# Optimization experiments

Measured on AMD Instinct MI355X. Metric: run time of the kernel, lower is better.

## Reference

```python
import jax, jax.numpy as jnp
import numpy as np

N_NODES = 5200    # max node index bounded by EW_weight length (5200)
N_INCID = 5200    # hyperedge_index.size(1), bounded by EW_weight length
N_HEDGES = 1000   # bounded by hyperedge_weight parameter length
N_DIM = 4096
NEG_SLOPE = 0.01  # torch.nn.LeakyReLU() default


def setup_inputs() -> dict:
    key = jax.random.key(0)
    k1, k2, k3, k4, k5, k6 = jax.random.split(key, 6)
    node_idx = jax.random.randint(k1, (N_INCID,), 0, N_NODES, dtype=jnp.int32)
    edge_idx = jax.random.randint(k2, (N_INCID,), 0, N_HEDGES, dtype=jnp.int32)
    edge_idx = edge_idx.at[-1].set(N_HEDGES - 1)  # ensure num_edges = max+1 = N_HEDGES (static)
    hyperedge_index = jnp.stack([node_idx, edge_idx], axis=0)
    features = jax.random.normal(k3, (N_NODES, N_DIM), dtype=jnp.float32)
    hyperedge_type = jnp.round(jax.random.uniform(k4, (N_HEDGES, 1), dtype=jnp.float32))
    return {
        "features": features,
        "hyperedge_index": hyperedge_index,
        "hyperedge_type": hyperedge_type,
        "hyperedge_weight": jnp.ones((1000,), jnp.float32),
        "hyperedge_attr1": jax.random.uniform(k5, (N_DIM,), dtype=jnp.float32),
        "hyperedge_attr2": jax.random.uniform(k6, (N_DIM,), dtype=jnp.float32),
        "EW_weight": jnp.ones((5200,), jnp.float32),
        "bias": jnp.zeros((N_DIM,), jnp.float32),
    }


def reference(features, hyperedge_index, hyperedge_type, hyperedge_weight,
              hyperedge_attr1, hyperedge_attr2, EW_weight, bias):
    node_idx = hyperedge_index[0]  # [E] node index of each incidence
    edge_idx = hyperedge_index[1]  # [E] hyperedge index of each incidence
    E = node_idx.shape[0]

    hw = hyperedge_weight[:N_HEDGES]   # hgnn slices param to num_edges
    norm = EW_weight[:E]               # hgnn slices param to E, passed as EW_weight

    # hyperedge_attr is computed but unused (use_attention=False in source)
    _ = hyperedge_attr1 * hyperedge_type + hyperedge_attr2 * (1.0 - hyperedge_type)

    # D: node-degree normalization (sum of incident hyperedge weights per node)
    D = jax.ops.segment_sum(hw[edge_idx], node_idx, num_segments=N_NODES)
    Dinv = jnp.where(D == 0, 0.0, 1.0 / D)
    # B: hyperedge normalization (sum of EW weights of member nodes per edge)
    B = jax.ops.segment_sum(norm[node_idx], edge_idx, num_segments=N_HEDGES)
    Binv = jnp.where(B == 0, 0.0, 1.0 / B)

    # Stage 1: node -> hyperedge (flow source_to_target), message = B_e * x_v
    msg1 = Binv[edge_idx][:, None] * features[node_idx]           # [E, F]
    edge_out = jax.ops.segment_sum(msg1, edge_idx, num_segments=N_HEDGES)  # [num_edges, F]

    # Stage 2: hyperedge -> node (flow target_to_source), message = D_v * e_feat
    msg2 = Dinv[node_idx][:, None] * edge_out[edge_idx]           # [E, F]
    node_out = jax.ops.segment_sum(msg2, node_idx, num_segments=N_NODES)   # [N, F]

    node_out = node_out + bias
    return (jax.nn.leaky_relu(node_out, NEG_SLOPE),
            jax.nn.leaky_relu(edge_out, NEG_SLOPE))
```

## Files before the change

### kernel.cpp

```cpp
#include <hip/hip_runtime.h>

#define NN 5200
#define NI 5200
#define NH 1000
#define ND 4096
#define SLOPE 0.01f


__global__ void count_k(const int* __restrict__ hidx, int* __restrict__ ecnt,
                        int* __restrict__ ncnt) {
    int i = blockIdx.x * blockDim.x + threadIdx.x;
    if (i < NI) {
        atomicAdd(&ncnt[hidx[i]], 1);
        atomicAdd(&ecnt[hidx[NI + i]], 1);
    }
}

__device__ void scan_one(const int* __restrict__ cnt, int* __restrict__ off,
                         int* __restrict__ fill, int n, int* lds) {
    int t = threadIdx.x;
    int per = (n + 1023) >> 10;
    int base = t * per;
    int s = 0;
    for (int i = 0; i < per; ++i) {
        int id = base + i;
        if (id < n) s += cnt[id];
    }
    lds[t] = s;
    __syncthreads();
    for (int d = 1; d < 1024; d <<= 1) {
        int v = (t >= d) ? lds[t - d] : 0;
        __syncthreads();
        lds[t] += v;
        __syncthreads();
    }
    int total = lds[1023];
    int run = (t == 0) ? 0 : lds[t - 1];
    for (int i = 0; i < per; ++i) {
        int id = base + i;
        if (id < n) { off[id] = run; fill[id] = run; run += cnt[id]; }
    }
    if (t == 0) off[n] = total;
}

__global__ void __launch_bounds__(1024) scan_k(const int* ecnt, const int* ncnt,
                                               int* eoff, int* noff,
                                               int* efill, int* nfill) {
    __shared__ int lds[1024];
    scan_one(ecnt, eoff, efill, NH, lds);
    __syncthreads();
    scan_one(ncnt, noff, nfill, NN, lds);
}

__global__ void scatter_k(const int* __restrict__ hidx, int* __restrict__ efill,
                          int* __restrict__ nfill, int* __restrict__ elist,
                          int* __restrict__ nlist) {
    int i = blockIdx.x * blockDim.x + threadIdx.x;
    if (i < NI) {
        int p = atomicAdd(&nfill[hidx[i]], 1);
        nlist[p] = i;
        int q = atomicAdd(&efill[hidx[NI + i]], 1);
        elist[q] = i;
    }
}


__global__ void __launch_bounds__(256) edge_k(const float* __restrict__ feat,
        const int* __restrict__ hidx, const float* __restrict__ eww,
        const int* __restrict__ eoff, const int* __restrict__ elist,
        float* __restrict__ eraw) {
    int h = blockIdx.x, t = threadIdx.x;
    int s = eoff[h], e = eoff[h + 1];
    __shared__ float sBinv;
    if (t == 0) {
        float B = 0.f;
        for (int i = s; i < e; ++i) B += eww[hidx[elist[i]]];
        sBinv = (B == 0.f) ? 0.f : 1.f / B;
    }
    __syncthreads();
    float binv = sBinv;
    float4 a0 = make_float4(0, 0, 0, 0), a1 = a0, a2 = a0, a3 = a0;
    for (int i = s; i < e; ++i) {
        const float4* row = (const float4*)(feat + (size_t)hidx[elist[i]] * ND);
        float4 v0 = row[t], v1 = row[t + 256], v2 = row[t + 512], v3 = row[t + 768];
        a0.x += v0.x; a0.y += v0.y; a0.z += v0.z; a0.w += v0.w;
        a1.x += v1.x; a1.y += v1.y; a1.z += v1.z; a1.w += v1.w;
        a2.x += v2.x; a2.y += v2.y; a2.z += v2.z; a2.w += v2.w;
        a3.x += v3.x; a3.y += v3.y; a3.z += v3.z; a3.w += v3.w;
    }
    a0.x *= binv; a0.y *= binv; a0.z *= binv; a0.w *= binv;
    a1.x *= binv; a1.y *= binv; a1.z *= binv; a1.w *= binv;
    a2.x *= binv; a2.y *= binv; a2.z *= binv; a2.w *= binv;
    a3.x *= binv; a3.y *= binv; a3.z *= binv; a3.w *= binv;
    float4* out = (float4*)(eraw + (size_t)h * ND);
    out[t] = a0; out[t + 256] = a1; out[t + 512] = a2; out[t + 768] = a3;
}

__global__ void __launch_bounds__(256) node_k(const float* __restrict__ eraw,
        const int* __restrict__ hidx, const float* __restrict__ hw,
        const float* __restrict__ bias, const int* __restrict__ noff,
        const int* __restrict__ nlist, float* __restrict__ nout) {
    int n = blockIdx.x, t = threadIdx.x;
    int s = noff[n], e = noff[n + 1];
    __shared__ float sDinv;
    if (t == 0) {
        float D = 0.f;
        for (int i = s; i < e; ++i) D += hw[hidx[NI + nlist[i]]];
        sDinv = (D == 0.f) ? 0.f : 1.f / D;
    }
    __syncthreads();
    float dinv = sDinv;
    float4 a0 = make_float4(0, 0, 0, 0), a1 = a0, a2 = a0, a3 = a0;
    for (int i = s; i < e; ++i) {
        const float4* row = (const float4*)(eraw + (size_t)hidx[NI + nlist[i]] * ND);
        float4 v0 = row[t], v1 = row[t + 256], v2 = row[t + 512], v3 = row[t + 768];
        a0.x += v0.x; a0.y += v0.y; a0.z += v0.z; a0.w += v0.w;
        a1.x += v1.x; a1.y += v1.y; a1.z += v1.z; a1.w += v1.w;
        a2.x += v2.x; a2.y += v2.y; a2.z += v2.z; a2.w += v2.w;
        a3.x += v3.x; a3.y += v3.y; a3.z += v3.z; a3.w += v3.w;
    }
    const float4* b4 = (const float4*)bias;
    float4* out = (float4*)(nout + (size_t)n * ND);
#define FIN(ak, idx)                                                     \
    {                                                                    \
        float4 b = b4[idx];                                              \
        float4 v;                                                        \
        v.x = dinv * ak.x + b.x; v.y = dinv * ak.y + b.y;                \
        v.z = dinv * ak.z + b.z; v.w = dinv * ak.w + b.w;                \
        v.x = v.x >= 0.f ? v.x : SLOPE * v.x;                            \
        v.y = v.y >= 0.f ? v.y : SLOPE * v.y;                            \
        v.z = v.z >= 0.f ? v.z : SLOPE * v.z;                            \
        v.w = v.w >= 0.f ? v.w : SLOPE * v.w;                            \
        out[idx] = v;                                                    \
    }
    FIN(a0, t);
    FIN(a1, t + 256);
    FIN(a2, t + 512);
    FIN(a3, t + 768);
#undef FIN
}

__global__ void relu_k(float4* __restrict__ p, int n4) {
    int i = blockIdx.x * blockDim.x + threadIdx.x;
    if (i < n4) {
        float4 v = p[i];
        v.x = v.x >= 0.f ? v.x : SLOPE * v.x;
        v.y = v.y >= 0.f ? v.y : SLOPE * v.y;
        v.z = v.z >= 0.f ? v.z : SLOPE * v.z;
        v.w = v.w >= 0.f ? v.w : SLOPE * v.w;
        p[i] = v;
    }
}

extern "C" void kernel_launch(void* const* d_in, const int* in_sizes, int n_in,
                              void* d_out, int out_size, void* d_ws, size_t ws_size,
                              hipStream_t stream) {
    const float* feat = (const float*)d_in[0];
    const int* hidx   = (const int*)d_in[1];
    const float* hw   = (const float*)d_in[3];
    const float* eww  = (const float*)d_in[6];
    const float* bias = (const float*)d_in[7];

    float* nout = (float*)d_out;
    float* eraw = nout + (size_t)NN * ND;

    int* ws    = (int*)d_ws;
    int* ecnt  = ws;
    int* ncnt  = ecnt + NH;
    int* eoff  = ncnt + NN;
    int* noff  = eoff + NH + 1;
    int* efill = noff + NN + 1;
    int* nfill = efill + NH;
    int* elist = nfill + NN;
    int* nlist = elist + NI;

    hipMemsetAsync(ecnt, 0, (size_t)(NH + NN) * sizeof(int), stream);
    count_k<<<(NI + 255) / 256, 256, 0, stream>>>(hidx, ecnt, ncnt);
    scan_k<<<1, 1024, 0, stream>>>(ecnt, ncnt, eoff, noff, efill, nfill);
    scatter_k<<<(NI + 255) / 256, 256, 0, stream>>>(hidx, efill, nfill, elist, nlist);
    edge_k<<<NH, 256, 0, stream>>>(feat, hidx, eww, eoff, elist, eraw);
    node_k<<<NN, 256, 0, stream>>>(eraw, hidx, hw, bias, noff, nlist, nout);
    relu_k<<<(NH * ND / 4 + 255) / 256, 256, 0, stream>>>((float4*)eraw, NH * ND / 4);
}
```

Before: 213.6 us.

## Fuse edge LeakyReLU into edge kernel, precompute degree sums, split rows across blocks

Degree sums B and D are now computed with float atomics in the count kernel rather than by a serial loop in one thread per block. The CSR lists store the neighbor index directly, which removes one level of indirection. Each row is split across 4 blocks of 256 threads with one float4 each, for more parallelism and occupancy. The separate LeakyReLU pass over edge output is removed: the edge kernel writes activated values, and the node kernel undoes the activation by multiplying negatives by 100. That inversion can differ slightly from the reference in floating point, and the float atomics make B and D order-dependent.

```diff
diff --git a/kernel.cpp b/kernel.cpp
--- a/kernel.cpp
+++ b/kernel.cpp
@@ -5,14 +5,21 @@
 #define NH 1000
 #define ND 4096
 #define SLOPE 0.01f
+#define INV_SLOPE 100.0f
 
 
-__global__ void count_k(const int* __restrict__ hidx, int* __restrict__ ecnt,
-                        int* __restrict__ ncnt) {
+__global__ void count_k(const int* __restrict__ hidx, const float* __restrict__ hw,
+                        const float* __restrict__ eww,
+                        int* __restrict__ ecnt, int* __restrict__ ncnt,
+                        float* __restrict__ Bsum, float* __restrict__ Dsum) {
     int i = blockIdx.x * blockDim.x + threadIdx.x;
     if (i < NI) {
-        atomicAdd(&ncnt[hidx[i]], 1);
-        atomicAdd(&ecnt[hidx[NI + i]], 1);
+        int n = hidx[i];
+        int h = hidx[NI + i];
+        atomicAdd(&ncnt[n], 1);
+        atomicAdd(&ecnt[h], 1);
+        atomicAdd(&Dsum[n], hw[h]);
+        atomicAdd(&Bsum[h], eww[n]);
     }
 }
 
@@ -57,99 +64,76 @@
                           int* __restrict__ nlist) {
     int i = blockIdx.x * blockDim.x + threadIdx.x;
     if (i < NI) {
-        int p = atomicAdd(&nfill[hidx[i]], 1);
-        nlist[p] = i;
-        int q = atomicAdd(&efill[hidx[NI + i]], 1);
-        elist[q] = i;
+        int n = hidx[i];
+        int h = hidx[NI + i];
+        int p = atomicAdd(&nfill[n], 1);
+        nlist[p] = h;
+        int q = atomicAdd(&efill[h], 1);
+        elist[q] = n;
     }
 }
 
+__global__ void __launch_bounds__(256) edge_k(const float* __restrict__ feat,
+        const int* __restrict__ eoff, const int* __restrict__ elist,
+        const float* __restrict__ Bsum, float* __restrict__ eout) {
+    int bid = blockIdx.x;
+    int h = bid >> 2;
+    int col = ((bid & 3) << 8) + threadIdx.x;
+    int s = eoff[h], e = eoff[h + 1];
+    float B = Bsum[h];
+    float binv = (B == 0.f) ? 0.f : 1.f / B;
 
-__global__ void __launch_bounds__(256) edge_k(const float* __restrict__ feat,
-        const int* __restrict__ hidx, const float* __restrict__ eww,
-        const int* __restrict__ eoff, const int* __restrict__ elist,
-        float* __restrict__ eraw) {
-    int h = blockIdx.x, t = threadIdx.x;
-    int s = eoff[h], e = eoff[h + 1];
-    __shared__ float sBinv;
-    if (t == 0) {
-        float B = 0.f;
-        for (int i = s; i < e; ++i) B += eww[hidx[elist[i]]];
-        sBinv = (B == 0.f) ? 0.f : 1.f / B;
+    float4 acc = make_float4(0.f, 0.f, 0.f, 0.f);
+    int i = s;
+    int nid = (i < e) ? elist[i] : 0;
+    for (; i < e; ++i) {
+        int nid_next = (i + 1 < e) ? elist[i + 1] : 0;
+        float4 v = ((const float4*)(feat + (size_t)nid * ND))[col];
+        acc.x += v.x; acc.y += v.y; acc.z += v.z; acc.w += v.w;
+        nid = nid_next;
     }
-    __syncthreads();
-    float binv = sBinv;
-    float4 a0 = make_float4(0, 0, 0, 0), a1 = a0, a2 = a0, a3 = a0;
-    for (int i = s; i < e; ++i) {
-        const float4* row = (const float4*)(feat + (size_t)hidx[elist[i]] * ND);
-        float4 v0 = row[t], v1 = row[t + 256], v2 = row[t + 512], v3 = row[t + 768];
-        a0.x += v0.x; a0.y += v0.y; a0.z += v0.z; a0.w += v0.w;
-        a1.x += v1.x; a1.y += v1.y; a1.z += v1.z; a1.w += v1.w;
-        a2.x += v2.x; a2.y += v2.y; a2.z += v2.z; a2.w += v2.w;
-        a3.x += v3.x; a3.y += v3.y; a3.z += v3.z; a3.w += v3.w;
-    }
-    a0.x *= binv; a0.y *= binv; a0.z *= binv; a0.w *= binv;
-    a1.x *= binv; a1.y *= binv; a1.z *= binv; a1.w *= binv;
-    a2.x *= binv; a2.y *= binv; a2.z *= binv; a2.w *= binv;
-    a3.x *= binv; a3.y *= binv; a3.z *= binv; a3.w *= binv;
-    float4* out = (float4*)(eraw + (size_t)h * ND);
-    out[t] = a0; out[t + 256] = a1; out[t + 512] = a2; out[t + 768] = a3;
+    float4 r;
+    r.x = binv * acc.x; r.y = binv * acc.y; r.z = binv * acc.z; r.w = binv * acc.w;
+    r.x = r.x >= 0.f ? r.x : SLOPE * r.x;
+    r.y = r.y >= 0.f ? r.y : SLOPE * r.y;
+    r.z = r.z >= 0.f ? r.z : SLOPE * r.z;
+    r.w = r.w >= 0.f ? r.w : SLOPE * r.w;
+    ((float4*)(eout + (size_t)h * ND))[col] = r;
 }
 
-__global__ void __launch_bounds__(256) node_k(const float* __restrict__ eraw,
-        const int* __restrict__ hidx, const float* __restrict__ hw,
-        const float* __restrict__ bias, const int* __restrict__ noff,
-        const int* __restrict__ nlist, float* __restrict__ nout) {
-    int n = blockIdx.x, t = threadIdx.x;
+__global__ void __launch_bounds__(256) node_k(const float* __restrict__ eout,
+        const int* __restrict__ noff, const int* __restrict__ nlist,
+        const float* __restrict__ Dsum, const float* __restrict__ bias,
+        float* __restrict__ nout) {
+    int bid = blockIdx.x;
+    int n = bid >> 2;
+    int col = ((bid & 3) << 8) + threadIdx.x;
     int s = noff[n], e = noff[n + 1];
-    __shared__ float sDinv;
-    if (t == 0) {
-        float D = 0.f;
-        for (int i = s; i < e; ++i) D += hw[hidx[NI + nlist[i]]];
-        sDinv = (D == 0.f) ? 0.f : 1.f / D;
+    float D = Dsum[n];
+    float dinv = (D == 0.f) ? 0.f : 1.f / D;
+
+    float4 acc = make_float4(0.f, 0.f, 0.f, 0.f);
+    int i = s;
+    int hid = (i < e) ? nlist[i] : 0;
+    for (; i < e; ++i) {
+        int hid_next = (i + 1 < e) ? nlist[i + 1] : 0;
+        float4 v = ((const float4*)(eout + (size_t)hid * ND))[col];
+        v.x = v.x >= 0.f ? v.x : INV_SLOPE * v.x;
+        v.y = v.y >= 0.f ? v.y : INV_SLOPE * v.y;
+        v.z = v.z >= 0.f ? v.z : INV_SLOPE * v.z;
+        v.w = v.w >= 0.f ? v.w : INV_SLOPE * v.w;
+        acc.x += v.x; acc.y += v.y; acc.z += v.z; acc.w += v.w;
+        hid = hid_next;
     }
-    __syncthreads();
-    float dinv = sDinv;
-    float4 a0 = make_float4(0, 0, 0, 0), a1 = a0, a2 = a0, a3 = a0;
-    for (int i = s; i < e; ++i) {
-        const float4* row = (const float4*)(eraw + (size_t)hidx[NI + nlist[i]] * ND);
-        float4 v0 = row[t], v1 = row[t + 256], v2 = row[t + 512], v3 = row[t + 768];
-        a0.x += v0.x; a0.y += v0.y; a0.z += v0.z; a0.w += v0.w;
-        a1.x += v1.x; a1.y += v1.y; a1.z += v1.z; a1.w += v1.w;
-        a2.x += v2.x; a2.y += v2.y; a2.z += v2.z; a2.w += v2.w;
-        a3.x += v3.x; a3.y += v3.y; a3.z += v3.z; a3.w += v3.w;
-    }
-    const float4* b4 = (const float4*)bias;
-    float4* out = (float4*)(nout + (size_t)n * ND);
-#define FIN(ak, idx)                                                     \
-    {                                                                    \
-        float4 b = b4[idx];                                              \
-        float4 v;                                                        \
-        v.x = dinv * ak.x + b.x; v.y = dinv * ak.y + b.y;                \
-        v.z = dinv * ak.z + b.z; v.w = dinv * ak.w + b.w;                \
-        v.x = v.x >= 0.f ? v.x : SLOPE * v.x;                            \
-        v.y = v.y >= 0.f ? v.y : SLOPE * v.y;                            \
-        v.z = v.z >= 0.f ? v.z : SLOPE * v.z;                            \
-        v.w = v.w >= 0.f ? v.w : SLOPE * v.w;                            \
-        out[idx] = v;                                                    \
-    }
-    FIN(a0, t);
-    FIN(a1, t + 256);
-    FIN(a2, t + 512);
-    FIN(a3, t + 768);
-#undef FIN
-}
-
-__global__ void relu_k(float4* __restrict__ p, int n4) {
-    int i = blockIdx.x * blockDim.x + threadIdx.x;
-    if (i < n4) {
-        float4 v = p[i];
-        v.x = v.x >= 0.f ? v.x : SLOPE * v.x;
-        v.y = v.y >= 0.f ? v.y : SLOPE * v.y;
-        v.z = v.z >= 0.f ? v.z : SLOPE * v.z;
-        v.w = v.w >= 0.f ? v.w : SLOPE * v.w;
-        p[i] = v;
-    }
+    float4 b = ((const float4*)bias)[col];
+    float4 v;
+    v.x = dinv * acc.x + b.x; v.y = dinv * acc.y + b.y;
+    v.z = dinv * acc.z + b.z; v.w = dinv * acc.w + b.w;
+    v.x = v.x >= 0.f ? v.x : SLOPE * v.x;
+    v.y = v.y >= 0.f ? v.y : SLOPE * v.y;
+    v.z = v.z >= 0.f ? v.z : SLOPE * v.z;
+    v.w = v.w >= 0.f ? v.w : SLOPE * v.w;
+    ((float4*)(nout + (size_t)n * ND))[col] = v;
 }
 
 extern "C" void kernel_launch(void* const* d_in, const int* in_sizes, int n_in,
@@ -162,23 +146,24 @@
     const float* bias = (const float*)d_in[7];
 
     float* nout = (float*)d_out;
-    float* eraw = nout + (size_t)NN * ND;
+    float* eout = nout + (size_t)NN * ND;
 
-    int* ws    = (int*)d_ws;
-    int* ecnt  = ws;
-    int* ncnt  = ecnt + NH;
-    int* eoff  = ncnt + NN;
-    int* noff  = eoff + NH + 1;
-    int* efill = noff + NN + 1;
-    int* nfill = efill + NH;
-    int* elist = nfill + NN;
-    int* nlist = elist + NI;
+    int* ws      = (int*)d_ws;
+    int* ecnt    = ws;
+    int* ncnt    = ecnt + NH;
+    float* Bsum  = (float*)(ncnt + NN);
+    float* Dsum  = Bsum + NH;
+    int* eoff    = (int*)(Dsum + NN);
+    int* noff    = eoff + NH + 1;
+    int* efill   = noff + NN + 1;
+    int* nfill   = efill + NH;
+    int* elist   = nfill + NN;
+    int* nlist   = elist + NI;
 
-    hipMemsetAsync(ecnt, 0, (size_t)(NH + NN) * sizeof(int), stream);
-    count_k<<<(NI + 255) / 256, 256, 0, stream>>>(hidx, ecnt, ncnt);
+    hipMemsetAsync(ecnt, 0, (size_t)2 * (NH + NN) * sizeof(int), stream);
+    count_k<<<(NI + 255) / 256, 256, 0, stream>>>(hidx, hw, eww, ecnt, ncnt, Bsum, Dsum);
     scan_k<<<1, 1024, 0, stream>>>(ecnt, ncnt, eoff, noff, efill, nfill);
     scatter_k<<<(NI + 255) / 256, 256, 0, stream>>>(hidx, efill, nfill, elist, nlist);
-    edge_k<<<NH, 256, 0, stream>>>(feat, hidx, eww, eoff, elist, eraw);
-    node_k<<<NN, 256, 0, stream>>>(eraw, hidx, hw, bias, noff, nlist, nout);
-    relu_k<<<(NH * ND / 4 + 255) / 256, 256, 0, stream>>>((float4*)eraw, NH * ND / 4);
+    edge_k<<<NH * 4, 256, 0, stream>>>(feat, eoff, elist, Bsum, eout);
+    node_k<<<NN * 4, 256, 0, stream>>>(eout, noff, nlist, Dsum, bias, nout);
 }
```

New measurement: 199.6 us. -6.5%, faster.
